# Kernel tuning notes

Measured on AMD Instinct MI355X. Metric: run time of the kernel, lower is better.

Reference implementation:

```python
import jax, jax.numpy as jnp
import numpy as np
from jax import lax

DIM = 192
HEADS = 8
B, H, W = 2, 256, 256
EPS = 1e-12  # F.normalize default eps


def conv1x1(x, w):
    # x: [b, ci, h, w], w: [co, ci]
    return jnp.einsum('oi,bihw->bohw', w, x)


def dwconv3x3(x, w):
    # depthwise 3x3, SAME padding; w: [c, 1, 3, 3]
    c = x.shape[1]
    return lax.conv_general_dilated(
        x, w, window_strides=(1, 1), padding='SAME',
        dimension_numbers=('NCHW', 'OIHW', 'NCHW'),
        feature_group_count=c)


def l2norm(x):
    # F.normalize over last axis
    n = jnp.sqrt(jnp.sum(x * x, axis=-1, keepdims=True))
    return x / jnp.maximum(n, EPS)


def setup_inputs() -> dict:
    key = jax.random.key(0)
    ks = jax.random.split(key, 8)
    s = 0.02
    return {
        'x': jax.random.normal(ks[0], (B, DIM, H, W), jnp.float32),
        'x_ref': jax.random.normal(ks[1], (B, DIM, H, W), jnp.float32),
        'wq': jax.random.normal(ks[2], (DIM, DIM), jnp.float32) * s,
        'wq_dw': jax.random.normal(ks[3], (DIM, 1, 3, 3), jnp.float32) * s,
        'wkv': jax.random.normal(ks[4], (2 * DIM, DIM), jnp.float32) * s,
        'wkv_dw': jax.random.normal(ks[5], (2 * DIM, 1, 3, 3), jnp.float32) * s,
        'wproj': jax.random.normal(ks[6], (DIM, DIM), jnp.float32) * s,
        'temperature': jnp.ones((HEADS, 1, 1), jnp.float32),
    }


def reference(x, x_ref, wq, wq_dw, wkv, wkv_dw, wproj, temperature):
    b, c, h, w = x.shape
    ch = c // HEADS  # channels per head
    hw = h * w

    q = dwconv3x3(conv1x1(x, wq), wq_dw)            # [b, c, h, w]
    kv = dwconv3x3(conv1x1(x_ref, wkv), wkv_dw)      # [b, 2c, h, w]
    k, v = jnp.split(kv, 2, axis=1)

    q = q.reshape(b, HEADS, ch, hw)
    k = k.reshape(b, HEADS, ch, hw)
    v = v.reshape(b, HEADS, ch, hw)

    q = l2norm(q)
    k = l2norm(k)

    # channel-wise attention: [b, head, ch, ch]
    attn = jnp.einsum('bhcn,bhdn->bhcd', q, k) * temperature
    attn = jax.nn.softmax(attn, axis=-1)
    out = jnp.einsum('bhcd,bhdn->bhcn', attn, v)     # [b, head, ch, hw]

    out = out.reshape(b, c, h, w)
    out = conv1x1(out, wproj)
    return out
```

## Files before the change

kernel.cpp:

```cpp
#include <hip/hip_runtime.h>
#include <hip/hip_bf16.h>

#define B_ 2
#define C_ 192
#define HEADS_ 8
#define CH_ 24
#define H_ 256
#define W_ 256
#define HW_ 65536


using bf16x8 = __attribute__((ext_vector_type(8))) __bf16;
using f32x4  = __attribute__((ext_vector_type(4))) float;

__device__ __forceinline__ float b2f_us(unsigned short u) {
    return __uint_as_float(((unsigned)u) << 16);
}
__device__ __forceinline__ unsigned short f2bf(float f) {
    union { __hip_bfloat16 b; unsigned short u; } cv;
    cv.b = __float2bfloat16(f);
    return cv.u;
}

__global__ __launch_bounds__(256) void convert_w(
    const float* __restrict__ wq, const float* __restrict__ wkv,
    unsigned short* __restrict__ wqbf, unsigned short* __restrict__ wkvbf)
{
    int i = blockIdx.x * 256 + threadIdx.x;
    const float* src; unsigned short* dst; int qd;
    if (i < 9216) { src = wq;  dst = wqbf;  qd = i; }
    else          { src = wkv; dst = wkvbf; qd = i - 9216; }
    float4 v = *(const float4*)(src + (size_t)qd * 4);
    ushort4 u;
    u.x = f2bf(v.x); u.y = f2bf(v.y); u.z = f2bf(v.z); u.w = f2bf(v.w);
    *(ushort4*)(dst + (size_t)qd * 4) = u;
}

#define BPITCH 200
template<bool B_F32, bool OUT_F32>
__global__ __launch_bounds__(256) void gemm_mfma(
    const unsigned short* __restrict__ A, long a_bstride,
    const void* __restrict__ Bv, void* __restrict__ Outv, int outC)
{
    const int nb = blockIdx.x * 64;
    const int mt = blockIdx.y;
    const int b  = blockIdx.z;
    const int t  = threadIdx.x;

    __shared__ unsigned short Bl[64 * BPITCH];

    const unsigned short* Ab = A + (size_t)b * a_bstride + (size_t)mt * 192 * 192;

    const int w = t >> 6, l = t & 63, li = l & 15, q = l >> 4;

    f32x4 acc[3][4];
#pragma unroll
    for (int mi = 0; mi < 3; mi++)
#pragma unroll
        for (int ni = 0; ni < 4; ni++)
            acc[mi][ni] = (f32x4){0.f, 0.f, 0.f, 0.f};

    const int p0 = (t & 15) * 4;
    const int kp = t >> 4;

#pragma unroll
    for (int kc = 0; kc < 6; kc++) {
        const int k = kc * 32 + kp * 2;
        unsigned int packed[4];
        if (B_F32) {
            const float* Bb = (const float*)Bv + (size_t)b * 192 * HW_;
            float4 r0 = *(const float4*)(Bb + (size_t)k * HW_ + nb + p0);
            float4 r1 = *(const float4*)(Bb + (size_t)(k + 1) * HW_ + nb + p0);
            packed[0] = (unsigned)f2bf(r0.x) | ((unsigned)f2bf(r1.x) << 16);
            packed[1] = (unsigned)f2bf(r0.y) | ((unsigned)f2bf(r1.y) << 16);
            packed[2] = (unsigned)f2bf(r0.z) | ((unsigned)f2bf(r1.z) << 16);
            packed[3] = (unsigned)f2bf(r0.w) | ((unsigned)f2bf(r1.w) << 16);
        } else {
            const unsigned short* Bb = (const unsigned short*)Bv + (size_t)b * 192 * HW_;
            ushort4 r0 = *(const ushort4*)(Bb + (size_t)k * HW_ + nb + p0);
            ushort4 r1 = *(const ushort4*)(Bb + (size_t)(k + 1) * HW_ + nb + p0);
            packed[0] = (unsigned)r0.x | ((unsigned)r1.x << 16);
            packed[1] = (unsigned)r0.y | ((unsigned)r1.y << 16);
            packed[2] = (unsigned)r0.z | ((unsigned)r1.z << 16);
            packed[3] = (unsigned)r0.w | ((unsigned)r1.w << 16);
        }
#pragma unroll
        for (int c = 0; c < 4; c++) {
            int p = p0 + c;
            int rB = ((p & 3) << 4) | (p >> 2);
            *(unsigned int*)&Bl[rB * BPITCH + k] = packed[c];
        }
    }
    __syncthreads();

#pragma unroll
    for (int kc = 0; kc < 6; kc++) {
        bf16x8 af[3], bfr[4];
#pragma unroll
        for (int mi = 0; mi < 3; mi++)
            af[mi] = *(const bf16x8*)(Ab + (size_t)(w * 48 + mi * 16 + li) * 192
                                         + kc * 32 + q * 8);
#pragma unroll
        for (int ni = 0; ni < 4; ni++)
            bfr[ni] = *(const bf16x8*)&Bl[(ni * 16 + li) * BPITCH + kc * 32 + q * 8];
#pragma unroll
        for (int mi = 0; mi < 3; mi++)
#pragma unroll
            for (int ni = 0; ni < 4; ni++)
                acc[mi][ni] = __builtin_amdgcn_mfma_f32_16x16x32_bf16(
                    af[mi], bfr[ni], acc[mi][ni], 0, 0, 0);
    }

    if (OUT_F32) {
        float* Ob = (float*)Outv + ((size_t)b * outC + (size_t)mt * 192) * HW_;
#pragma unroll
        for (int mi = 0; mi < 3; mi++)
#pragma unroll
            for (int r = 0; r < 4; r++) {
                int o = w * 48 + mi * 16 + q * 4 + r;
                float4 vv;
                vv.x = acc[mi][0][r]; vv.y = acc[mi][1][r];
                vv.z = acc[mi][2][r]; vv.w = acc[mi][3][r];
                *(float4*)(Ob + (size_t)o * HW_ + nb + 4 * li) = vv;
            }
    } else {
        unsigned short* Ob = (unsigned short*)Outv + ((size_t)b * outC + (size_t)mt * 192) * HW_;
#pragma unroll
        for (int mi = 0; mi < 3; mi++)
#pragma unroll
            for (int r = 0; r < 4; r++) {
                int o = w * 48 + mi * 16 + q * 4 + r;
                ushort4 u;
                u.x = f2bf(acc[mi][0][r]); u.y = f2bf(acc[mi][1][r]);
                u.z = f2bf(acc[mi][2][r]); u.w = f2bf(acc[mi][3][r]);
                *(ushort4*)(Ob + (size_t)o * HW_ + nb + 4 * li) = u;
            }
    }
}

#define VYG 4
__global__ __launch_bounds__(256) void dwconv_v(
    const __hip_bfloat16* __restrict__ tmpKV, const float* __restrict__ wkv_dw,
    __hip_bfloat16* __restrict__ V)
{
    const int y0 = blockIdx.x * VYG, cg = blockIdx.y, b = blockIdx.z;
    const int t = threadIdx.x;
    const int c = cg * 32 + (t >> 3);
    const int x0 = (t & 7) * 32;
    const unsigned short* base =
        (const unsigned short*)(tmpKV + ((size_t)b * 2 * C_ + C_ + c) * HW_);
    const float* wp = wkv_dw + (size_t)(C_ + c) * 9;
    float wgt[9];
#pragma unroll
    for (int i = 0; i < 9; i++) wgt[i] = wp[i];

    for (int yi = 0; yi < VYG; yi++) {
        const int y = y0 + yi;
        float o[32];
#pragma unroll
        for (int i = 0; i < 32; i++) o[i] = 0.f;

#pragma unroll
        for (int dy = -1; dy <= 1; dy++) {
            int yy = y + dy;
            if ((unsigned)yy >= 256u) continue;
            const unsigned short* r = base + yy * W_;
            float v[34];
            v[0]  = (x0 > 0) ? b2f_us(r[x0 - 1]) : 0.f;
            v[33] = (x0 + 32 < 256) ? b2f_us(r[x0 + 32]) : 0.f;
            const uint4* r4 = (const uint4*)(r + x0);
#pragma unroll
            for (int m = 0; m < 4; m++) {
                uint4 raw = r4[m];
                unsigned u;
                u = raw.x; v[1 + 8*m + 0] = __uint_as_float(u << 16); v[1 + 8*m + 1] = __uint_as_float(u & 0xffff0000u);
                u = raw.y; v[1 + 8*m + 2] = __uint_as_float(u << 16); v[1 + 8*m + 3] = __uint_as_float(u & 0xffff0000u);
                u = raw.z; v[1 + 8*m + 4] = __uint_as_float(u << 16); v[1 + 8*m + 5] = __uint_as_float(u & 0xffff0000u);
                u = raw.w; v[1 + 8*m + 6] = __uint_as_float(u << 16); v[1 + 8*m + 7] = __uint_as_float(u & 0xffff0000u);
            }
            float w0 = wgt[3 * (dy + 1) + 0];
            float w1 = wgt[3 * (dy + 1) + 1];
            float w2 = wgt[3 * (dy + 1) + 2];
#pragma unroll
            for (int i = 0; i < 32; i++)
                o[i] += v[i] * w0 + v[i + 1] * w1 + v[i + 2] * w2;
        }
        unsigned short* dst = (unsigned short*)V + ((size_t)b * C_ + c) * HW_ + y * W_ + x0;
#pragma unroll
        for (int m = 0; m < 4; m++) {
            uint4 pk;
            pk.x = (unsigned)f2bf(o[8*m + 0]) | ((unsigned)f2bf(o[8*m + 1]) << 16);
            pk.y = (unsigned)f2bf(o[8*m + 2]) | ((unsigned)f2bf(o[8*m + 3]) << 16);
            pk.z = (unsigned)f2bf(o[8*m + 4]) | ((unsigned)f2bf(o[8*m + 5]) << 16);
            pk.w = (unsigned)f2bf(o[8*m + 6]) | ((unsigned)f2bf(o[8*m + 7]) << 16);
            *(uint4*)(dst + 8 * m) = pk;
        }
    }
}

#define PADB 264
#define YG 4
__global__ __launch_bounds__(256) void dw_qk_gram(
    const __hip_bfloat16* __restrict__ tmpQ,
    const __hip_bfloat16* __restrict__ tmpKV,
    const float* __restrict__ wq_dw, const float* __restrict__ wkv_dw,
    float* __restrict__ G, float* __restrict__ sq, float* __restrict__ sk)
{
    const int y0 = blockIdx.x * YG, h = blockIdx.y, b = blockIdx.z;
    const int t = threadIdx.x;

    __shared__ unsigned short Qs[CH_ * PADB];
    __shared__ unsigned short Ks[CH_ * PADB];
    __shared__ float sqs[CH_], sks[CH_];

    if (t < CH_) { sqs[t] = 0.f; sks[t] = 0.f; }

    const int w = t >> 6, l = t & 63, li = l & 15, q = l >> 4;
    const int tr = w >> 1, tc = w & 1;
    int ar = tr * 16 + li; if (ar > 23) ar = 23;
    int br = tc * 16 + li; if (br > 23) br = 23;
    const unsigned short* arow = &Qs[ar * PADB];
    const unsigned short* brow = &Ks[br * PADB];
    f32x4 acc = (f32x4){0.f, 0.f, 0.f, 0.f};

    __syncthreads();

    for (int yi = 0; yi < YG; yi++) {
        const int y = y0 + yi;

        for (int u = t; u < 384; u += 256) {
            const int tens = (u >= 192);
            const int rem = u - tens * 192;
            const int c = rem >> 3;
            const int x0 = (rem & 7) * 32;
            const unsigned short* base = tens
                ? (const unsigned short*)(tmpKV + ((size_t)b * 2 * C_ + h * CH_ + c) * HW_)
                : (const unsigned short*)(tmpQ  + ((size_t)b * C_     + h * CH_ + c) * HW_);
            const float* wp = (tens ? wkv_dw : wq_dw) + (size_t)(h * CH_ + c) * 9;

            float o[32];
#pragma unroll
            for (int i = 0; i < 32; i++) o[i] = 0.f;

#pragma unroll
            for (int dy = -1; dy <= 1; dy++) {
                int yy = y + dy;
                if ((unsigned)yy >= 256u) continue;
                const unsigned short* r = base + yy * W_;
                float v[34];
                v[0]  = (x0 > 0) ? b2f_us(r[x0 - 1]) : 0.f;
                v[33] = (x0 + 32 < 256) ? b2f_us(r[x0 + 32]) : 0.f;
                const uint4* r4 = (const uint4*)(r + x0);
#pragma unroll
                for (int m = 0; m < 4; m++) {
                    uint4 raw = r4[m];
                    unsigned uu;
                    uu = raw.x; v[1 + 8*m + 0] = __uint_as_float(uu << 16); v[1 + 8*m + 1] = __uint_as_float(uu & 0xffff0000u);
                    uu = raw.y; v[1 + 8*m + 2] = __uint_as_float(uu << 16); v[1 + 8*m + 3] = __uint_as_float(uu & 0xffff0000u);
                    uu = raw.z; v[1 + 8*m + 4] = __uint_as_float(uu << 16); v[1 + 8*m + 5] = __uint_as_float(uu & 0xffff0000u);
                    uu = raw.w; v[1 + 8*m + 6] = __uint_as_float(uu << 16); v[1 + 8*m + 7] = __uint_as_float(uu & 0xffff0000u);
                }
                float w0 = wp[3 * (dy + 1) + 0];
                float w1 = wp[3 * (dy + 1) + 1];
                float w2 = wp[3 * (dy + 1) + 2];
#pragma unroll
                for (int i = 0; i < 32; i++)
                    o[i] += v[i] * w0 + v[i + 1] * w1 + v[i + 2] * w2;
            }

            float s = 0.f;
#pragma unroll
            for (int i = 0; i < 32; i++) s += o[i] * o[i];
            atomicAdd(tens ? &sks[c] : &sqs[c], s);

            unsigned short* dst = (tens ? Ks : Qs) + c * PADB + x0;
#pragma unroll
            for (int m = 0; m < 4; m++) {
                uint4 pk;
                pk.x = (unsigned)f2bf(o[8*m + 0]) | ((unsigned)f2bf(o[8*m + 1]) << 16);
                pk.y = (unsigned)f2bf(o[8*m + 2]) | ((unsigned)f2bf(o[8*m + 3]) << 16);
                pk.z = (unsigned)f2bf(o[8*m + 4]) | ((unsigned)f2bf(o[8*m + 5]) << 16);
                pk.w = (unsigned)f2bf(o[8*m + 6]) | ((unsigned)f2bf(o[8*m + 7]) << 16);
                *(uint4*)(dst + 8 * m) = pk;
            }
        }
        __syncthreads();

#pragma unroll
        for (int ks = 0; ks < 8; ks++) {
            bf16x8 af = *(const bf16x8*)&arow[ks * 32 + q * 8];
            bf16x8 bf = *(const bf16x8*)&brow[ks * 32 + q * 8];
            acc = __builtin_amdgcn_mfma_f32_16x16x32_bf16(af, bf, acc, 0, 0, 0);
        }
        __syncthreads();
    }

    if (t < CH_) {
        atomicAdd(&sq[b * C_ + h * CH_ + t], sqs[t]);
        atomicAdd(&sk[b * C_ + h * CH_ + t], sks[t]);
    }

    float* Gb = G + (size_t)(b * HEADS_ + h) * CH_ * CH_;
    const int col = tc * 16 + li;
    if (col < CH_) {
#pragma unroll
        for (int r = 0; r < 4; r++) {
            int row = tr * 16 + q * 4 + r;
            if (row < CH_)
                atomicAdd(&Gb[row * CH_ + col], acc[r]);
        }
    }
}

__global__ __launch_bounds__(192) void softmax_proj(
    const float* __restrict__ G, const float* __restrict__ sq,
    const float* __restrict__ sk, const float* __restrict__ temperature,
    const float* __restrict__ wproj, unsigned short* __restrict__ Mbf)
{
    const int h = blockIdx.x, b = blockIdx.y, t = threadIdx.x;
    __shared__ float attn[CH_][CH_];
    __shared__ float rk[CH_];
    const float* Gb = G + (size_t)(b * HEADS_ + h) * CH_ * CH_;
    if (t < CH_)
        rk[t] = 1.f / fmaxf(sqrtf(sk[b * C_ + h * CH_ + t]), 1e-12f);
    __syncthreads();
    if (t < CH_) {
        float rq = 1.f / fmaxf(sqrtf(sq[b * C_ + h * CH_ + t]), 1e-12f);
        float tempv = temperature[h];
        float row[CH_];
        float mx = -1e30f;
        for (int d = 0; d < CH_; d++) {
            row[d] = Gb[t * CH_ + d] * rq * rk[d] * tempv;
            mx = fmaxf(mx, row[d]);
        }
        float s = 0.f;
        for (int d = 0; d < CH_; d++) { row[d] = __expf(row[d] - mx); s += row[d]; }
        float inv = 1.f / s;
        for (int d = 0; d < CH_; d++) attn[t][d] = row[d] * inv;
    }
    __syncthreads();
    const int o = t;
    float wrow[CH_];
    for (int c = 0; c < CH_; c++) wrow[c] = wproj[o * C_ + h * CH_ + c];
    for (int d = 0; d < CH_; d++) {
        float s = 0.f;
        for (int c = 0; c < CH_; c++) s += wrow[c] * attn[c][d];
        Mbf[((size_t)b * C_ + o) * C_ + h * CH_ + d] = f2bf(s);
    }
}

extern "C" void kernel_launch(void* const* d_in, const int* in_sizes, int n_in,
                              void* d_out, int out_size, void* d_ws, size_t ws_size,
                              hipStream_t stream)
{
    const float* x           = (const float*)d_in[0];
    const float* x_ref       = (const float*)d_in[1];
    const float* wq          = (const float*)d_in[2];
    const float* wq_dw       = (const float*)d_in[3];
    const float* wkv         = (const float*)d_in[4];
    const float* wkv_dw      = (const float*)d_in[5];
    const float* wproj       = (const float*)d_in[6];
    const float* temperature = (const float*)d_in[7];
    float* out = (float*)d_out;

    char* ws = (char*)d_ws;
    __hip_bfloat16* tmpQ  = (__hip_bfloat16*)(ws);
    __hip_bfloat16* tmpKV = (__hip_bfloat16*)(ws + 50331648);
    __hip_bfloat16* tmpV  = (__hip_bfloat16*)(ws);
    float* G  = (float*)(ws + 150994944);
    float* sq = (float*)(ws + 151031808);
    float* sk = (float*)(ws + 151033344);
    unsigned short* wqbf  = (unsigned short*)(ws + 151034880);
    unsigned short* wkvbf = (unsigned short*)(ws + 151108608);
    unsigned short* Mbf   = (unsigned short*)(ws + 151034880);

    hipMemsetAsync(G, 0, 36864 + 1536 + 1536, stream);

    convert_w<<<dim3(108), 256, 0, stream>>>(wq, wkv, wqbf, wkvbf);
    gemm_mfma<true, false><<<dim3(HW_ / 64, 1, B_), 256, 0, stream>>>(
        wqbf, 0, x, tmpQ, 192);
    gemm_mfma<true, false><<<dim3(HW_ / 64, 2, B_), 256, 0, stream>>>(
        wkvbf, 0, x_ref, tmpKV, 384);
    dw_qk_gram<<<dim3(H_ / YG, HEADS_, B_), 256, 0, stream>>>(
        tmpQ, tmpKV, wq_dw, wkv_dw, G, sq, sk);
    softmax_proj<<<dim3(HEADS_, B_), 192, 0, stream>>>(
        G, sq, sk, temperature, wproj, Mbf);
    dwconv_v<<<dim3(H_ / VYG, 6, B_), 256, 0, stream>>>(tmpKV, wkv_dw, tmpV);
    gemm_mfma<false, true><<<dim3(HW_ / 64, 1, B_), 256, 0, stream>>>(
        Mbf, 192 * 192, tmpV, out, 192);
}
```

Baseline: 447.0 us.

## Software-pipeline 1x1-conv GEMM with triple-buffered LDS k-chunks and two N tiles per block

```diff
diff --git a/kernel.cpp b/kernel.cpp
--- a/kernel.cpp
+++ b/kernel.cpp
@@ -36,22 +36,69 @@
     *(ushort4*)(dst + (size_t)qd * 4) = u;
 }
 
-#define BPITCH 200
-template<bool B_F32, bool OUT_F32>
+template<int NT, bool B_F32, bool OUT_F32>
 __global__ __launch_bounds__(256) void gemm_mfma(
     const unsigned short* __restrict__ A, long a_bstride,
     const void* __restrict__ Bv, void* __restrict__ Outv, int outC)
 {
-    const int nb = blockIdx.x * 64;
+    constexpr int S = 6 * NT;
+    const int nb0 = blockIdx.x * (64 * NT);
     const int mt = blockIdx.y;
     const int b  = blockIdx.z;
     const int t  = threadIdx.x;
 
-    __shared__ unsigned short Bl[64 * BPITCH];
+    __shared__ unsigned short Bl[3][64 * 40];
 
     const unsigned short* Ab = A + (size_t)b * a_bstride + (size_t)mt * 192 * 192;
-
     const int w = t >> 6, l = t & 63, li = l & 15, q = l >> 4;
+    const int p0 = (t & 15) * 4;
+    const int kp = t >> 4;
+
+    const float* Bf = (const float*)Bv + (size_t)b * 192 * HW_;
+    const unsigned short* Bh = (const unsigned short*)Bv + (size_t)b * 192 * HW_;
+
+    float4  rf[2][2];
+    ushort4 rh[2][2];
+    bf16x8  af[2][3];
+
+    auto LOADB = [&](int c, int set) {
+        const int ti = c / 6, kc = c % 6;
+        const size_t off = (size_t)(kc * 32 + kp * 2) * HW_ + nb0 + ti * 64 + p0;
+        if constexpr (B_F32) {
+            rf[set][0] = *(const float4*)(Bf + off);
+            rf[set][1] = *(const float4*)(Bf + off + HW_);
+        } else {
+            rh[set][0] = *(const ushort4*)(Bh + off);
+            rh[set][1] = *(const ushort4*)(Bh + off + HW_);
+        }
+    };
+    auto CVTW = [&](int c, int set) {
+        unsigned pk2[4];
+        if constexpr (B_F32) {
+            pk2[0] = (unsigned)f2bf(rf[set][0].x) | ((unsigned)f2bf(rf[set][1].x) << 16);
+            pk2[1] = (unsigned)f2bf(rf[set][0].y) | ((unsigned)f2bf(rf[set][1].y) << 16);
+            pk2[2] = (unsigned)f2bf(rf[set][0].z) | ((unsigned)f2bf(rf[set][1].z) << 16);
+            pk2[3] = (unsigned)f2bf(rf[set][0].w) | ((unsigned)f2bf(rf[set][1].w) << 16);
+        } else {
+            pk2[0] = (unsigned)rh[set][0].x | ((unsigned)rh[set][1].x << 16);
+            pk2[1] = (unsigned)rh[set][0].y | ((unsigned)rh[set][1].y << 16);
+            pk2[2] = (unsigned)rh[set][0].z | ((unsigned)rh[set][1].z << 16);
+            pk2[3] = (unsigned)rh[set][0].w | ((unsigned)rh[set][1].w << 16);
+        }
+        unsigned short* dst = &Bl[c % 3][kp * 2];
+#pragma unroll
+        for (int c4 = 0; c4 < 4; c4++) {
+            int p = p0 + c4;
+            int rB = ((p & 3) << 4) | (p >> 2);
+            *(unsigned int*)&dst[rB * 40] = pk2[c4];
+        }
+    };
+    auto AFLOAD = [&](int kc, int set) {
+#pragma unroll
+        for (int mi = 0; mi < 3; mi++)
+            af[set][mi] = *(const bf16x8*)(Ab + (size_t)(w * 48 + mi * 16 + li) * 192
+                                              + kc * 32 + q * 8);
+    };
 
     f32x4 acc[3][4];
 #pragma unroll
@@ -60,81 +107,66 @@
         for (int ni = 0; ni < 4; ni++)
             acc[mi][ni] = (f32x4){0.f, 0.f, 0.f, 0.f};
 
-    const int p0 = (t & 15) * 4;
-    const int kp = t >> 4;
-
-#pragma unroll
-    for (int kc = 0; kc < 6; kc++) {
-        const int k = kc * 32 + kp * 2;
-        unsigned int packed[4];
-        if (B_F32) {
-            const float* Bb = (const float*)Bv + (size_t)b * 192 * HW_;
-            float4 r0 = *(const float4*)(Bb + (size_t)k * HW_ + nb + p0);
-            float4 r1 = *(const float4*)(Bb + (size_t)(k + 1) * HW_ + nb + p0);
-            packed[0] = (unsigned)f2bf(r0.x) | ((unsigned)f2bf(r1.x) << 16);
-            packed[1] = (unsigned)f2bf(r0.y) | ((unsigned)f2bf(r1.y) << 16);
-            packed[2] = (unsigned)f2bf(r0.z) | ((unsigned)f2bf(r1.z) << 16);
-            packed[3] = (unsigned)f2bf(r0.w) | ((unsigned)f2bf(r1.w) << 16);
-        } else {
-            const unsigned short* Bb = (const unsigned short*)Bv + (size_t)b * 192 * HW_;
-            ushort4 r0 = *(const ushort4*)(Bb + (size_t)k * HW_ + nb + p0);
-            ushort4 r1 = *(const ushort4*)(Bb + (size_t)(k + 1) * HW_ + nb + p0);
-            packed[0] = (unsigned)r0.x | ((unsigned)r1.x << 16);
-            packed[1] = (unsigned)r0.y | ((unsigned)r1.y << 16);
-            packed[2] = (unsigned)r0.z | ((unsigned)r1.z << 16);
-            packed[3] = (unsigned)r0.w | ((unsigned)r1.w << 16);
-        }
-#pragma unroll
-        for (int c = 0; c < 4; c++) {
-            int p = p0 + c;
-            int rB = ((p & 3) << 4) | (p >> 2);
-            *(unsigned int*)&Bl[rB * BPITCH + k] = packed[c];
-        }
-    }
-    __syncthreads();
-
-#pragma unroll
-    for (int kc = 0; kc < 6; kc++) {
-        bf16x8 af[3], bfr[4];
-#pragma unroll
-        for (int mi = 0; mi < 3; mi++)
-            af[mi] = *(const bf16x8*)(Ab + (size_t)(w * 48 + mi * 16 + li) * 192
-                                         + kc * 32 + q * 8);
+    LOADB(0, 0);
+    LOADB(1, 1);
+    AFLOAD(0, 0);
+    CVTW(0, 0);
+    LOADB(2, 0);
+
+#pragma unroll
+    for (int s = 0; s < S; s++) {
+        if (s + 1 < S) {
+            CVTW(s + 1, (s + 1) & 1);
+            AFLOAD((s + 1) % 6, (s + 1) & 1);
+        }
+        if (s + 3 < S) LOADB(s + 3, (s + 1) & 1);
+        asm volatile("s_waitcnt lgkmcnt(0)" ::: "memory");
+        __builtin_amdgcn_s_barrier();
+
+        bf16x8 bfr[4];
 #pragma unroll
         for (int ni = 0; ni < 4; ni++)
-            bfr[ni] = *(const bf16x8*)&Bl[(ni * 16 + li) * BPITCH + kc * 32 + q * 8];
+            bfr[ni] = *(const bf16x8*)&Bl[s % 3][(ni * 16 + li) * 40 + q * 8];
 #pragma unroll
         for (int mi = 0; mi < 3; mi++)
 #pragma unroll
             for (int ni = 0; ni < 4; ni++)
                 acc[mi][ni] = __builtin_amdgcn_mfma_f32_16x16x32_bf16(
-                    af[mi], bfr[ni], acc[mi][ni], 0, 0, 0);
-    }
-
-    if (OUT_F32) {
-        float* Ob = (float*)Outv + ((size_t)b * outC + (size_t)mt * 192) * HW_;
-#pragma unroll
-        for (int mi = 0; mi < 3; mi++)
-#pragma unroll
-            for (int r = 0; r < 4; r++) {
-                int o = w * 48 + mi * 16 + q * 4 + r;
-                float4 vv;
-                vv.x = acc[mi][0][r]; vv.y = acc[mi][1][r];
-                vv.z = acc[mi][2][r]; vv.w = acc[mi][3][r];
-                *(float4*)(Ob + (size_t)o * HW_ + nb + 4 * li) = vv;
+                    af[s & 1][mi], bfr[ni], acc[mi][ni], 0, 0, 0);
+
+        if ((s % 6) == 5) {
+            const int nb = nb0 + (s / 6) * 64;
+            if (OUT_F32) {
+                float* Ob = (float*)Outv + ((size_t)b * outC + (size_t)mt * 192) * HW_;
+#pragma unroll
+                for (int mi = 0; mi < 3; mi++)
+#pragma unroll
+                    for (int r = 0; r < 4; r++) {
+                        int o = w * 48 + mi * 16 + q * 4 + r;
+                        float4 vv;
+                        vv.x = acc[mi][0][r]; vv.y = acc[mi][1][r];
+                        vv.z = acc[mi][2][r]; vv.w = acc[mi][3][r];
+                        *(float4*)(Ob + (size_t)o * HW_ + nb + 4 * li) = vv;
+                    }
+            } else {
+                unsigned short* Ob = (unsigned short*)Outv + ((size_t)b * outC + (size_t)mt * 192) * HW_;
+#pragma unroll
+                for (int mi = 0; mi < 3; mi++)
+#pragma unroll
+                    for (int r = 0; r < 4; r++) {
+                        int o = w * 48 + mi * 16 + q * 4 + r;
+                        ushort4 u;
+                        u.x = f2bf(acc[mi][0][r]); u.y = f2bf(acc[mi][1][r]);
+                        u.z = f2bf(acc[mi][2][r]); u.w = f2bf(acc[mi][3][r]);
+                        *(ushort4*)(Ob + (size_t)o * HW_ + nb + 4 * li) = u;
+                    }
             }
-    } else {
-        unsigned short* Ob = (unsigned short*)Outv + ((size_t)b * outC + (size_t)mt * 192) * HW_;
-#pragma unroll
-        for (int mi = 0; mi < 3; mi++)
-#pragma unroll
-            for (int r = 0; r < 4; r++) {
-                int o = w * 48 + mi * 16 + q * 4 + r;
-                ushort4 u;
-                u.x = f2bf(acc[mi][0][r]); u.y = f2bf(acc[mi][1][r]);
-                u.z = f2bf(acc[mi][2][r]); u.w = f2bf(acc[mi][3][r]);
-                *(ushort4*)(Ob + (size_t)o * HW_ + nb + 4 * li) = u;
-            }
+#pragma unroll
+            for (int mi = 0; mi < 3; mi++)
+#pragma unroll
+                for (int ni = 0; ni < 4; ni++)
+                    acc[mi][ni] = (f32x4){0.f, 0.f, 0.f, 0.f};
+        }
     }
 }
 
@@ -377,15 +409,15 @@
     hipMemsetAsync(G, 0, 36864 + 1536 + 1536, stream);
 
     convert_w<<<dim3(108), 256, 0, stream>>>(wq, wkv, wqbf, wkvbf);
-    gemm_mfma<true, false><<<dim3(HW_ / 64, 1, B_), 256, 0, stream>>>(
+    gemm_mfma<2, true, false><<<dim3(HW_ / 128, 1, B_), 256, 0, stream>>>(
         wqbf, 0, x, tmpQ, 192);
-    gemm_mfma<true, false><<<dim3(HW_ / 64, 2, B_), 256, 0, stream>>>(
+    gemm_mfma<2, true, false><<<dim3(HW_ / 128, 2, B_), 256, 0, stream>>>(
         wkvbf, 0, x_ref, tmpKV, 384);
     dw_qk_gram<<<dim3(H_ / YG, HEADS_, B_), 256, 0, stream>>>(
         tmpQ, tmpKV, wq_dw, wkv_dw, G, sq, sk);
     softmax_proj<<<dim3(HEADS_, B_), 192, 0, stream>>>(
         G, sq, sk, temperature, wproj, Mbf);
     dwconv_v<<<dim3(H_ / VYG, 6, B_), 256, 0, stream>>>(tmpKV, wkv_dw, tmpV);
-    gemm_mfma<false, true><<<dim3(HW_ / 64, 1, B_), 256, 0, stream>>>(
+    gemm_mfma<2, false, true><<<dim3(HW_ / 128, 1, B_), 256, 0, stream>>>(
         Mbf, 192 * 192, tmpV, out, 192);
 }
```

After: 445.7 us. About the same (-0.3%).
